# Kernel optimization log

Measured on AMD Instinct MI355X. Metric: run time of the kernel, lower is better.

## Reference

```python
import jax, jax.numpy as jnp
import numpy as np

ALPHA = 32.0 ** 2
EPS = 1e-5
SCALE = 64 ** (-0.5)  # dim_head ** -0.5
HEADS = 8


def stable_softmax(t, alpha=ALPHA):
    t = t / alpha
    t = t - jax.lax.stop_gradient(jnp.max(t, axis=-1, keepdims=True))
    return jax.nn.softmax(t * alpha, axis=-1)


def setup_inputs() -> dict:
    key = jax.random.key(0)
    k1, k2, k3 = jax.random.split(key, 3)
    dim, inner = 512, 8 * 64
    x = jax.random.normal(k1, (8, dim, 32, 32), dtype=jnp.float32)
    gamma = jnp.ones((1, dim, 1, 1), dtype=jnp.float32)
    # conv2d 1x1 weights, stored as [out_ch, in_ch]
    w_qkv = jax.random.normal(k2, (inner * 3, dim), dtype=jnp.float32) * (dim ** -0.5)
    w_out = jax.random.normal(k3, (dim, inner), dtype=jnp.float32) * (inner ** -0.5)
    return {"x": x, "gamma": gamma, "w_qkv": w_qkv, "w_out": w_out}


def reference(x, gamma, w_qkv, w_out):
    b, c, H, W = x.shape
    residual = x
    # LayerNormChan: normalize over channel dim (biased variance), scale by gamma
    mean = jnp.mean(x, axis=1, keepdims=True)
    var = jnp.var(x, axis=1, keepdims=True)
    xn = (x - mean) / jnp.sqrt(var + EPS) * gamma
    # 1x1 conv QKV projection
    qkv = jnp.einsum('oc,bchw->bohw', w_qkv, xn)
    q, k, v = jnp.split(qkv, 3, axis=1)
    n = H * W
    def to_heads(t):
        return t.reshape(b, HEADS, -1, n)  # b h c (x y)
    q, k, v = map(to_heads, (q, k, v))
    sim = jnp.einsum('bhci,bhcj->bhij', q, k) * SCALE
    attn = stable_softmax(sim)
    out = jnp.einsum('bhij,bhcj->bhci', attn, v)
    out = out.reshape(b, -1, H, W)  # b (h c) x y
    out = jnp.einsum('oc,bchw->bohw', w_out, out)
    return out + residual
```

## Files before the change

kernel.cpp:

```cpp
#include <hip/hip_runtime.h>
#include <hip/hip_bf16.h>

#define NDIM   512
#define NPOS   1024
#define NB     8
#define INNER  1536
#define DHEAD  64

typedef __attribute__((ext_vector_type(8))) short bf8v;
typedef __attribute__((ext_vector_type(4))) float f4v;

__device__ __forceinline__ f4v mfma16(bf8v a, bf8v b, f4v c) {
    return __builtin_amdgcn_mfma_f32_16x16x32_bf16(a, b, c, 0, 0, 0);
}

__device__ __forceinline__ unsigned short f2bs(float v) {
    __hip_bfloat16 h = __float2bfloat16(v);
    return *reinterpret_cast<unsigned short*>(&h);
}

__device__ __forceinline__ void gl_lds16(const unsigned short* g, unsigned short* l) {
    __builtin_amdgcn_global_load_lds(
        (const __attribute__((address_space(1))) void*)g,
        (__attribute__((address_space(3))) void*)l,
        16, 0, 0);
}

__global__ __launch_bounds__(256) void prep_kernel(
    const float* __restrict__ x, const float* __restrict__ gamma,
    const float* __restrict__ wq, const float* __restrict__ wo,
    unsigned short* __restrict__ xnT, unsigned short* __restrict__ wqb,
    unsigned short* __restrict__ wob)
{
    const int blk = blockIdx.x;
    const int t = threadIdx.x;
    if (blk >= 256) {
        const int n1 = INNER * NDIM / 4;
        int i = (blk - 256) * 256 + t;
        const float* src; unsigned short* dst; int j;
        if (i < n1) { src = wq; dst = wqb; j = i; }
        else        { src = wo; dst = wob; j = i - n1; }
        float4 v = ((const float4*)src)[j];
        ushort4 u;
        u.x = f2bs(v.x); u.y = f2bs(v.y); u.z = f2bs(v.z); u.w = f2bs(v.w);
        ((ushort4*)dst)[j] = u;
        return;
    }
    __shared__ float ssum[8][32];
    __shared__ float ssq[8][32];
    __shared__ float mean_s[32];
    __shared__ float rstd_s[32];
    __shared__ unsigned short tile[32][72];

    const int b = blk >> 5;
    const int n0 = (blk & 31) * 32;
    {
        const int ln = t & 31, cg = t >> 5;
        const float* xp = x + (size_t)b * NDIM * NPOS + n0 + ln;
        float s = 0.f, ss = 0.f;
#pragma unroll 8
        for (int c = cg * 64; c < cg * 64 + 64; ++c) {
            float v = xp[(size_t)c * NPOS];
            s += v; ss += v * v;
        }
        ssum[cg][ln] = s; ssq[cg][ln] = ss;
    }
    __syncthreads();
    if (t < 32) {
        float st = 0.f, sq = 0.f;
#pragma unroll
        for (int g = 0; g < 8; ++g) { st += ssum[g][t]; sq += ssq[g][t]; }
        float m = st * (1.0f / NDIM);
        float var = sq * (1.0f / NDIM) - m * m;
        mean_s[t] = m;
        rstd_s[t] = rsqrtf(var + 1e-5f);
    }
    __syncthreads();

    const int cl = t >> 2, nq = (t & 3) * 8;
    const int nr = t >> 3, ch = (t & 7) * 8;
    for (int c0 = 0; c0 < NDIM; c0 += 64) {
        const float g = gamma[c0 + cl];
        const float* xp = x + ((size_t)b * NDIM + c0 + cl) * NPOS + n0 + nq;
        float4 v0 = *(const float4*)(xp);
        float4 v1 = *(const float4*)(xp + 4);
        float4 m0 = *(const float4*)&mean_s[nq];
        float4 m1 = *(const float4*)&mean_s[nq + 4];
        float4 r0 = *(const float4*)&rstd_s[nq];
        float4 r1 = *(const float4*)&rstd_s[nq + 4];
        tile[nq + 0][cl] = f2bs((v0.x - m0.x) * r0.x * g);
        tile[nq + 1][cl] = f2bs((v0.y - m0.y) * r0.y * g);
        tile[nq + 2][cl] = f2bs((v0.z - m0.z) * r0.z * g);
        tile[nq + 3][cl] = f2bs((v0.w - m0.w) * r0.w * g);
        tile[nq + 4][cl] = f2bs((v1.x - m1.x) * r1.x * g);
        tile[nq + 5][cl] = f2bs((v1.y - m1.y) * r1.y * g);
        tile[nq + 6][cl] = f2bs((v1.z - m1.z) * r1.z * g);
        tile[nq + 7][cl] = f2bs((v1.w - m1.w) * r1.w * g);
        __syncthreads();
        unsigned short* dst = xnT + ((size_t)b * NPOS + n0 + nr) * NDIM + c0 + ch;
        *(uint4*)dst = *(const uint4*)&tile[nr][ch];
        __syncthreads();
    }
}

__global__ __launch_bounds__(256) void qkv_mfma_kernel(
    const unsigned short* __restrict__ wq, const unsigned short* __restrict__ xnT,
    unsigned short* __restrict__ qT, unsigned short* __restrict__ kT,
    unsigned short* __restrict__ vv)
{
    __shared__ __align__(16) unsigned short smem[4 * 64 * 72];

    const int b = blockIdx.z;
    const int m0 = blockIdx.y * 128, n0 = blockIdx.x * 128;
    const int t = threadIdx.x, w = t >> 6, lane = t & 63;
    const int l15 = lane & 15, quad = lane >> 4;
    const int wm = (w >> 1) * 64, wn = (w & 1) * 64;
    const unsigned short* Abase = wq + (size_t)m0 * NDIM;
    const unsigned short* Bbase = xnT + ((size_t)b * NPOS + n0) * NDIM;

    const int rl = lane >> 2, sl = lane & 3;
    const int cw = (sl ^ ((rl >> 1) & 3)) * 8;
    const int sA = (quad ^ ((l15 >> 1) & 3)) * 8;

    f4v acc[4][4];
#pragma unroll
    for (int i = 0; i < 4; ++i)
#pragma unroll
        for (int j = 0; j < 4; ++j) { acc[i][j][0]=0.f; acc[i][j][1]=0.f; acc[i][j][2]=0.f; acc[i][j][3]=0.f; }

#pragma unroll
    for (int e = 0; e < 2; ++e) {
        const int seg = w * 2 + e;
        const int r = seg * 16 + rl;
        gl_lds16(Abase + (size_t)r * NDIM + cw, smem + seg * 512);
        gl_lds16(Bbase + (size_t)r * NDIM + cw, smem + 4096 + seg * 512);
    }

    for (int k0 = 0; k0 < NDIM; k0 += 32) {
        const int cur = (k0 >> 5) & 1;
        unsigned short* At = smem + cur * 8192;
        unsigned short* Bt = At + 4096;
        __syncthreads();
        if (k0 + 32 < NDIM) {
            unsigned short* An = smem + (cur ^ 1) * 8192;
#pragma unroll
            for (int e = 0; e < 2; ++e) {
                const int seg = w * 2 + e;
                const int r = seg * 16 + rl;
                gl_lds16(Abase + (size_t)r * NDIM + k0 + 32 + cw, An + seg * 512);
                gl_lds16(Bbase + (size_t)r * NDIM + k0 + 32 + cw, An + 4096 + seg * 512);
            }
        }
        bf8v af[4], bfr[4];
#pragma unroll
        for (int ms = 0; ms < 4; ++ms) af[ms]  = *(const bf8v*)&At[(wm + ms * 16 + l15) * 32 + sA];
#pragma unroll
        for (int ns = 0; ns < 4; ++ns) bfr[ns] = *(const bf8v*)&Bt[(wn + ns * 16 + l15) * 32 + sA];
#pragma unroll
        for (int ms = 0; ms < 4; ++ms)
#pragma unroll
            for (int ns = 0; ns < 4; ++ns)
                acc[ms][ns] = mfma16(af[ms], bfr[ns], acc[ms][ns]);
    }
    __syncthreads();

    const int sec = m0 >> 9;
    const int om  = m0 & 511;
    if (sec == 2) {
        unsigned short (*bw)[72] = (unsigned short(*)[72])(smem + w * 64 * 72);
        unsigned short* vbase = vv + ((size_t)b * NDIM + om) * NPOS + n0;
#pragma unroll
        for (int ms = 0; ms < 4; ++ms)
#pragma unroll
            for (int ns = 0; ns < 4; ++ns)
#pragma unroll
                for (int r = 0; r < 4; ++r)
                    bw[ms * 16 + quad * 4 + r][ns * 16 + l15] = f2bs(acc[ms][ns][r]);
#pragma unroll
        for (int r2 = 0; r2 < 4; ++r2) {
            const int ml = r2 * 16 + (lane >> 2);
            unsigned short* dstr = vbase + (size_t)(wm + ml) * NPOS + wn + (lane & 3) * 8;
            *(uint4*)dstr        = *(const uint4*)&bw[ml][(lane & 3) * 8];
            *(uint4*)(dstr + 32) = *(const uint4*)&bw[ml][32 + (lane & 3) * 8];
        }
    } else {
        const float qsc = (sec == 0) ? 0.18033688f : 1.0f;
        unsigned short* gT = (sec == 0 ? qT : kT) + ((size_t)b * NPOS + n0) * NDIM + om;
        unsigned short (*bw)[72] = (unsigned short(*)[72])(smem + w * 64 * 72);
#pragma unroll
        for (int ms = 0; ms < 4; ++ms)
#pragma unroll
            for (int ns = 0; ns < 4; ++ns)
#pragma unroll
                for (int r = 0; r < 4; ++r)
                    bw[ns * 16 + l15][ms * 16 + quad * 4 + r] = f2bs(acc[ms][ns][r] * qsc);
#pragma unroll
        for (int r2 = 0; r2 < 4; ++r2) {
            const int nl = r2 * 16 + (lane >> 2);
            unsigned short* dstr = gT + (size_t)(wn + nl) * NDIM + wm + (lane & 3) * 8;
            *(uint4*)dstr        = *(const uint4*)&bw[nl][(lane & 3) * 8];
            *(uint4*)(dstr + 32) = *(const uint4*)&bw[nl][32 + (lane & 3) * 8];
        }
    }
}

__global__ __launch_bounds__(256, 2) void attn_mfma8_kernel(
    const unsigned short* __restrict__ qT, const unsigned short* __restrict__ kT,
    const unsigned short* __restrict__ vv, unsigned short* __restrict__ attnT)
{
    __shared__ __align__(16) unsigned short Kb[2][4096];
    __shared__ __align__(16) unsigned short Vb[2][4096];
    __shared__ __align__(16) unsigned short Ps[4][32][72];

    const int blk = blockIdx.x;
    const int xg = blk & 7, rr = blk >> 3;
    const int i0 = (rr & 7) * 128;
    const int bh = ((rr >> 3) << 3) | xg;
    const int b = bh >> 3, h = bh & 7;

    const int t = threadIdx.x, w = t >> 6, lane = t & 63;
    const int l15 = lane & 15, quad = lane >> 4;

    const unsigned short* kbase = kT + (size_t)b * NPOS * NDIM + h * DHEAD;
    const unsigned short* vbase = vv + ((size_t)b * NDIM + h * DHEAD) * NPOS;

    bf8v bq[2][2];
#pragma unroll
    for (int g = 0; g < 2; ++g) {
        const unsigned short* qrow =
            qT + ((size_t)b * NPOS + i0 + w * 32 + g * 16 + l15) * NDIM + h * DHEAD;
        bq[g][0] = *(const bf8v*)(qrow + quad * 8);
        bq[g][1] = *(const bf8v*)(qrow + 32 + quad * 8);
    }

    bf8v bones;
#pragma unroll
    for (int e = 0; e < 8; ++e) bones[e] = (short)0x3F80;

    const int rloc = lane >> 3;
    const int gch = ((lane & 7) ^ (rloc & 7)) * 8;
    const int sw0 = (quad ^ (l15 & 7)) * 8;
    const int sw1 = ((4 + quad) ^ (l15 & 7)) * 8;

#pragma unroll
    for (int e = 0; e < 2; ++e) {
        const int seg = w * 2 + e;
        const int row = seg * 8 + rloc;
        gl_lds16(kbase + (size_t)row * NDIM + gch, &Kb[0][seg * 512]);
        gl_lds16(vbase + (size_t)row * NPOS + gch, &Vb[0][seg * 512]);
    }

    f4v oc[2][5];
#pragma unroll
    for (int mg = 0; mg < 2; ++mg)
#pragma unroll
        for (int cs = 0; cs < 5; ++cs) { oc[mg][cs][0]=0.f; oc[mg][cs][1]=0.f; oc[mg][cs][2]=0.f; oc[mg][cs][3]=0.f; }

#pragma unroll 2
    for (int j0 = 0; j0 < NPOS; j0 += 64) {
        const int cur = (j0 >> 6) & 1, nxt = cur ^ 1;
        __syncthreads();
        if (j0 + 64 < NPOS) {
#pragma unroll
            for (int e = 0; e < 2; ++e) {
                const int seg = w * 2 + e;
                const int row = seg * 8 + rloc;
                gl_lds16(kbase + (size_t)(j0 + 64 + row) * NDIM + gch, &Kb[nxt][seg * 512]);
                gl_lds16(vbase + (size_t)row * NPOS + j0 + 64 + gch, &Vb[nxt][seg * 512]);
            }
        }

        f4v sacc[4][2];
        __builtin_amdgcn_s_setprio(1);
#pragma unroll
        for (int jt = 0; jt < 4; ++jt) {
            const int krow = (jt * 16 + l15) * 64;
            bf8v ak0 = *(const bf8v*)&Kb[cur][krow + sw0];
            bf8v ak1 = *(const bf8v*)&Kb[cur][krow + sw1];
#pragma unroll
            for (int g = 0; g < 2; ++g) {
                f4v s; s[0]=0.f; s[1]=0.f; s[2]=0.f; s[3]=0.f;
                s = mfma16(ak0, bq[g][0], s);
                sacc[jt][g] = mfma16(ak1, bq[g][1], s);
            }
        }
        __builtin_amdgcn_s_setprio(0);

#pragma unroll
        for (int jt = 0; jt < 4; ++jt)
#pragma unroll
            for (int g = 0; g < 2; ++g) {
                ushort4 pu;
                pu.x = f2bs(__builtin_amdgcn_exp2f(sacc[jt][g][0]));
                pu.y = f2bs(__builtin_amdgcn_exp2f(sacc[jt][g][1]));
                pu.z = f2bs(__builtin_amdgcn_exp2f(sacc[jt][g][2]));
                pu.w = f2bs(__builtin_amdgcn_exp2f(sacc[jt][g][3]));
                *(ushort4*)&Ps[w][g * 16 + l15][jt * 16 + quad * 4] = pu;
            }

        bf8v ap[2][2];
#pragma unroll
        for (int mg = 0; mg < 2; ++mg) {
            ap[mg][0] = *(const bf8v*)&Ps[w][mg * 16 + l15][quad * 8];
            ap[mg][1] = *(const bf8v*)&Ps[w][mg * 16 + l15][32 + quad * 8];
        }
        __builtin_amdgcn_s_setprio(1);
#pragma unroll
        for (int cs = 0; cs < 4; ++cs) {
            const int vrow = (cs * 16 + l15) * 64;
            bf8v bv0 = *(const bf8v*)&Vb[cur][vrow + sw0];
            bf8v bv1 = *(const bf8v*)&Vb[cur][vrow + sw1];
#pragma unroll
            for (int mg = 0; mg < 2; ++mg) {
                oc[mg][cs] = mfma16(ap[mg][0], bv0, oc[mg][cs]);
                oc[mg][cs] = mfma16(ap[mg][1], bv1, oc[mg][cs]);
            }
        }
#pragma unroll
        for (int mg = 0; mg < 2; ++mg) {
            oc[mg][4] = mfma16(ap[mg][0], bones, oc[mg][4]);
            oc[mg][4] = mfma16(ap[mg][1], bones, oc[mg][4]);
        }
        __builtin_amdgcn_s_setprio(0);
    }

#pragma unroll
    for (int mg = 0; mg < 2; ++mg) {
        float inv[4];
#pragma unroll
        for (int r = 0; r < 4; ++r) inv[r] = __builtin_amdgcn_rcpf(oc[mg][4][r]);
#pragma unroll
        for (int cs = 0; cs < 4; ++cs)
#pragma unroll
            for (int r = 0; r < 4; ++r)
                Ps[w][mg * 16 + quad * 4 + r][cs * 16 + l15] = f2bs(oc[mg][cs][r] * inv[r]);
    }
    {
        const int br = lane >> 1;
        const int bc = lane & 1;
        unsigned short* dst =
            attnT + ((size_t)b * NPOS + i0 + w * 32 + br) * NDIM + h * DHEAD;
#pragma unroll
        for (int q2 = 0; q2 < 4; ++q2)
            *(uint4*)(dst + (q2 * 2 + bc) * 8) = *(const uint4*)&Ps[w][br][(q2 * 2 + bc) * 8];
    }
}

__global__ __launch_bounds__(256) void out_mfma_kernel(
    const unsigned short* __restrict__ wo, const unsigned short* __restrict__ attnT,
    const float* __restrict__ x, float* __restrict__ outp)
{
    __shared__ __align__(16) unsigned short smem[12288];

    const int b = blockIdx.z;
    const int m0 = blockIdx.y * 64, n0 = blockIdx.x * 128;
    const int t = threadIdx.x, w = t >> 6, lane = t & 63;
    const int l15 = lane & 15, quad = lane >> 4;
    const int wm = (w >> 1) * 32, wn = (w & 1) * 64;
    const unsigned short* Abase = wo + (size_t)m0 * NDIM;
    const unsigned short* Bbase = attnT + ((size_t)b * NPOS + n0) * NDIM;

    const int rl = lane >> 2, sl = lane & 3;
    const int cw = (sl ^ ((rl >> 1) & 3)) * 8;
    const int sA = (quad ^ ((l15 >> 1) & 3)) * 8;

    f4v acc[2][4];
#pragma unroll
    for (int i = 0; i < 2; ++i)
#pragma unroll
        for (int j = 0; j < 4; ++j) { acc[i][j][0]=0.f; acc[i][j][1]=0.f; acc[i][j][2]=0.f; acc[i][j][3]=0.f; }

    {
        const int r = w * 16 + rl;
        gl_lds16(Abase + (size_t)r * NDIM + cw, smem + w * 512);
#pragma unroll
        for (int e = 0; e < 2; ++e) {
            const int seg = w * 2 + e;
            const int rb = seg * 16 + rl;
            gl_lds16(Bbase + (size_t)rb * NDIM + cw, smem + 2048 + seg * 512);
        }
    }

    for (int k0 = 0; k0 < NDIM; k0 += 32) {
        const int cur = (k0 >> 5) & 1;
        unsigned short* At = smem + cur * 6144;
        unsigned short* Bt = At + 2048;
        __syncthreads();
        if (k0 + 32 < NDIM) {
            unsigned short* An = smem + (cur ^ 1) * 6144;
            const int r = w * 16 + rl;
            gl_lds16(Abase + (size_t)r * NDIM + k0 + 32 + cw, An + w * 512);
#pragma unroll
            for (int e = 0; e < 2; ++e) {
                const int seg = w * 2 + e;
                const int rb = seg * 16 + rl;
                gl_lds16(Bbase + (size_t)rb * NDIM + k0 + 32 + cw, An + 2048 + seg * 512);
            }
        }
        bf8v af[2], bfr[4];
#pragma unroll
        for (int ms = 0; ms < 2; ++ms) af[ms]  = *(const bf8v*)&At[(wm + ms * 16 + l15) * 32 + sA];
#pragma unroll
        for (int ns = 0; ns < 4; ++ns) bfr[ns] = *(const bf8v*)&Bt[(wn + ns * 16 + l15) * 32 + sA];
#pragma unroll
        for (int ms = 0; ms < 2; ++ms)
#pragma unroll
            for (int ns = 0; ns < 4; ++ns)
                acc[ms][ns] = mfma16(af[ms], bfr[ns], acc[ms][ns]);
    }
    const float* xb = x + ((size_t)b * NDIM + m0) * NPOS + n0;
    float* ob = outp + ((size_t)b * NDIM + m0) * NPOS + n0;
#pragma unroll
    for (int ms = 0; ms < 2; ++ms)
#pragma unroll
        for (int r = 0; r < 4; ++r) {
            int m = wm + ms * 16 + quad * 4 + r;
#pragma unroll
            for (int ns = 0; ns < 4; ++ns) {
                int n = wn + ns * 16 + l15;
                ob[(size_t)m * NPOS + n] = acc[ms][ns][r] + xb[(size_t)m * NPOS + n];
            }
        }
}

extern "C" void kernel_launch(void* const* d_in, const int* in_sizes, int n_in,
                              void* d_out, int out_size, void* d_ws, size_t ws_size,
                              hipStream_t stream) {
    const float* x     = (const float*)d_in[0];
    const float* gamma = (const float*)d_in[1];
    const float* w_qkv = (const float*)d_in[2];
    const float* w_out = (const float*)d_in[3];
    float* out = (float*)d_out;

    unsigned short* xnT = (unsigned short*)d_ws;
    unsigned short* wqb = xnT + (size_t)NB * NPOS * NDIM;
    unsigned short* wob = wqb + (size_t)INNER * NDIM;
    unsigned short* qTw = wob + (size_t)NDIM * NDIM;
    unsigned short* kTw = qTw + (size_t)NB * NPOS * NDIM;
    unsigned short* vvw = kTw + (size_t)NB * NPOS * NDIM;
    unsigned short* aTw = vvw + (size_t)NB * NPOS * NDIM;

    prep_kernel<<<256 + (INNER * NDIM + NDIM * NDIM) / 4 / 256, 256, 0, stream>>>(
        x, gamma, w_qkv, w_out, xnT, wqb, wob);
    qkv_mfma_kernel<<<dim3(NPOS / 128, INNER / 128, NB), 256, 0, stream>>>(
        wqb, xnT, qTw, kTw, vvw);
    attn_mfma8_kernel<<<512, 256, 0, stream>>>(qTw, kTw, vvw, aTw);
    out_mfma_kernel<<<dim3(NPOS / 128, NDIM / 64, NB), 256, 0, stream>>>(wob, aTw, x, out);
}
```

Baseline: 133.8 us.

## Fuse all four stages into one cooperative persistent kernel with grid syncs

Replaces four separate kernel launches (layernorm/weight conversion, QKV GEMM, attention, output projection) with one cooperative kernel of 512 blocks that loops over each stage's work items and separates stages with grid.sync(). The goal is to remove launch gaps and tail idle time between kernels. In exchange, occupancy is capped at 2 blocks per CU, the QKV stage runs 768 tiles on 512 blocks, which leaves an imbalanced second wave, and each grid barrier has a cost. It falls back to the old multi-kernel path if the cooperative launch fails.

```diff
diff --git a/kernel.cpp b/kernel.cpp
--- a/kernel.cpp
+++ b/kernel.cpp
@@ -1,5 +1,8 @@
 #include <hip/hip_runtime.h>
 #include <hip/hip_bf16.h>
+#include <hip/hip_cooperative_groups.h>
+
+namespace cg = cooperative_groups;
 
 #define NDIM   512
 #define NPOS   1024
@@ -25,6 +28,413 @@
         (__attribute__((address_space(3))) void*)l,
         16, 0, 0);
 }
+
+__global__ __launch_bounds__(256, 2) void mega_kernel(
+    const float* __restrict__ x, const float* __restrict__ gamma,
+    const float* __restrict__ wq32, const float* __restrict__ wo32,
+    unsigned short* __restrict__ xnT, unsigned short* __restrict__ wqb,
+    unsigned short* __restrict__ wob, unsigned short* __restrict__ qT,
+    unsigned short* __restrict__ kT, unsigned short* __restrict__ vv,
+    unsigned short* __restrict__ attnT, float* __restrict__ outp)
+{
+    __shared__ __align__(16) unsigned char SM[51200];
+    cg::grid_group grid = cg::this_grid();
+    const int t = threadIdx.x;
+
+    {
+        float* ssum   = (float*)SM;
+        float* ssq    = (float*)(SM + 1024);
+        float* mean_s = (float*)(SM + 2048);
+        float* rstd_s = (float*)(SM + 2176);
+        unsigned short (*tile)[72] = (unsigned short(*)[72])(SM + 2304);
+        for (int vb = blockIdx.x; vb < 1280; vb += 512) {
+            if (vb >= 256) {
+                const int n1 = INNER * NDIM / 4;
+                int i = (vb - 256) * 256 + t;
+                const float* src; unsigned short* dst; int j;
+                if (i < n1) { src = wq32; dst = wqb; j = i; }
+                else        { src = wo32; dst = wob; j = i - n1; }
+                float4 v = ((const float4*)src)[j];
+                ushort4 u;
+                u.x = f2bs(v.x); u.y = f2bs(v.y); u.z = f2bs(v.z); u.w = f2bs(v.w);
+                ((ushort4*)dst)[j] = u;
+                continue;
+            }
+            const int b = vb >> 5;
+            const int n0 = (vb & 31) * 32;
+            {
+                const int ln = t & 31, cgp = t >> 5;
+                const float* xp = x + (size_t)b * NDIM * NPOS + n0 + ln;
+                float s = 0.f, ss = 0.f;
+#pragma unroll 8
+                for (int c = cgp * 64; c < cgp * 64 + 64; ++c) {
+                    float v = xp[(size_t)c * NPOS];
+                    s += v; ss += v * v;
+                }
+                ssum[cgp * 32 + ln] = s; ssq[cgp * 32 + ln] = ss;
+            }
+            __syncthreads();
+            if (t < 32) {
+                float st = 0.f, sq = 0.f;
+#pragma unroll
+                for (int g = 0; g < 8; ++g) { st += ssum[g * 32 + t]; sq += ssq[g * 32 + t]; }
+                float m = st * (1.0f / NDIM);
+                float var = sq * (1.0f / NDIM) - m * m;
+                mean_s[t] = m;
+                rstd_s[t] = rsqrtf(var + 1e-5f);
+            }
+            __syncthreads();
+
+            const int cl = t >> 2, nq = (t & 3) * 8;
+            const int nr = t >> 3, ch = (t & 7) * 8;
+            for (int c0 = 0; c0 < NDIM; c0 += 64) {
+                const float g = gamma[c0 + cl];
+                const float* xp = x + ((size_t)b * NDIM + c0 + cl) * NPOS + n0 + nq;
+                float4 v0 = *(const float4*)(xp);
+                float4 v1 = *(const float4*)(xp + 4);
+                float4 m0 = *(const float4*)&mean_s[nq];
+                float4 m1 = *(const float4*)&mean_s[nq + 4];
+                float4 r0 = *(const float4*)&rstd_s[nq];
+                float4 r1 = *(const float4*)&rstd_s[nq + 4];
+                tile[nq + 0][cl] = f2bs((v0.x - m0.x) * r0.x * g);
+                tile[nq + 1][cl] = f2bs((v0.y - m0.y) * r0.y * g);
+                tile[nq + 2][cl] = f2bs((v0.z - m0.z) * r0.z * g);
+                tile[nq + 3][cl] = f2bs((v0.w - m0.w) * r0.w * g);
+                tile[nq + 4][cl] = f2bs((v1.x - m1.x) * r1.x * g);
+                tile[nq + 5][cl] = f2bs((v1.y - m1.y) * r1.y * g);
+                tile[nq + 6][cl] = f2bs((v1.z - m1.z) * r1.z * g);
+                tile[nq + 7][cl] = f2bs((v1.w - m1.w) * r1.w * g);
+                __syncthreads();
+                unsigned short* dst = xnT + ((size_t)b * NPOS + n0 + nr) * NDIM + c0 + ch;
+                *(uint4*)dst = *(const uint4*)&tile[nr][ch];
+                __syncthreads();
+            }
+        }
+    }
+    grid.sync();
+
+    {
+        unsigned short* smem = (unsigned short*)SM;
+        const int w = t >> 6, lane = t & 63;
+        const int l15 = lane & 15, quad = lane >> 4;
+        const int wm = (w >> 1) * 64, wn = (w & 1) * 64;
+        const int rl = lane >> 2, sl = lane & 3;
+        const int cw = (sl ^ ((rl >> 1) & 3)) * 8;
+        const int sA = (quad ^ ((l15 >> 1) & 3)) * 8;
+
+        for (int vb = blockIdx.x; vb < 768; vb += 512) {
+            __syncthreads();
+            const int n0 = (vb & 7) * 128;
+            const int mi = vb >> 3;
+            const int b  = mi / 12;
+            const int m0 = (mi - b * 12) * 128;
+            const unsigned short* Abase = wqb + (size_t)m0 * NDIM;
+            const unsigned short* Bbase = xnT + ((size_t)b * NPOS + n0) * NDIM;
+
+            f4v acc[4][4];
+#pragma unroll
+            for (int i = 0; i < 4; ++i)
+#pragma unroll
+                for (int j = 0; j < 4; ++j) { acc[i][j][0]=0.f; acc[i][j][1]=0.f; acc[i][j][2]=0.f; acc[i][j][3]=0.f; }
+
+#pragma unroll
+            for (int e = 0; e < 2; ++e) {
+                const int seg = w * 2 + e;
+                const int r = seg * 16 + rl;
+                gl_lds16(Abase + (size_t)r * NDIM + cw, smem + seg * 512);
+                gl_lds16(Bbase + (size_t)r * NDIM + cw, smem + 4096 + seg * 512);
+            }
+
+            for (int k0 = 0; k0 < NDIM; k0 += 32) {
+                const int cur = (k0 >> 5) & 1;
+                unsigned short* At = smem + cur * 8192;
+                unsigned short* Bt = At + 4096;
+                __syncthreads();
+                if (k0 + 32 < NDIM) {
+                    unsigned short* An = smem + (cur ^ 1) * 8192;
+#pragma unroll
+                    for (int e = 0; e < 2; ++e) {
+                        const int seg = w * 2 + e;
+                        const int r = seg * 16 + rl;
+                        gl_lds16(Abase + (size_t)r * NDIM + k0 + 32 + cw, An + seg * 512);
+                        gl_lds16(Bbase + (size_t)r * NDIM + k0 + 32 + cw, An + 4096 + seg * 512);
+                    }
+                }
+                bf8v af[4], bfr[4];
+#pragma unroll
+                for (int ms = 0; ms < 4; ++ms) af[ms]  = *(const bf8v*)&At[(wm + ms * 16 + l15) * 32 + sA];
+#pragma unroll
+                for (int ns = 0; ns < 4; ++ns) bfr[ns] = *(const bf8v*)&Bt[(wn + ns * 16 + l15) * 32 + sA];
+#pragma unroll
+                for (int ms = 0; ms < 4; ++ms)
+#pragma unroll
+                    for (int ns = 0; ns < 4; ++ns)
+                        acc[ms][ns] = mfma16(af[ms], bfr[ns], acc[ms][ns]);
+            }
+            __syncthreads();
+
+            const int sec = m0 >> 9;
+            const int om  = m0 & 511;
+            if (sec == 2) {
+                unsigned short (*bw)[72] = (unsigned short(*)[72])(smem + w * 64 * 72);
+                unsigned short* vbase = vv + ((size_t)b * NDIM + om) * NPOS + n0;
+#pragma unroll
+                for (int ms = 0; ms < 4; ++ms)
+#pragma unroll
+                    for (int ns = 0; ns < 4; ++ns)
+#pragma unroll
+                        for (int r = 0; r < 4; ++r)
+                            bw[ms * 16 + quad * 4 + r][ns * 16 + l15] = f2bs(acc[ms][ns][r]);
+#pragma unroll
+                for (int r2 = 0; r2 < 4; ++r2) {
+                    const int ml = r2 * 16 + (lane >> 2);
+                    unsigned short* dstr = vbase + (size_t)(wm + ml) * NPOS + wn + (lane & 3) * 8;
+                    *(uint4*)dstr        = *(const uint4*)&bw[ml][(lane & 3) * 8];
+                    *(uint4*)(dstr + 32) = *(const uint4*)&bw[ml][32 + (lane & 3) * 8];
+                }
+            } else {
+                const float qsc = (sec == 0) ? 0.18033688f : 1.0f;
+                unsigned short* gT = (sec == 0 ? qT : kT) + ((size_t)b * NPOS + n0) * NDIM + om;
+                unsigned short (*bw)[72] = (unsigned short(*)[72])(smem + w * 64 * 72);
+#pragma unroll
+                for (int ms = 0; ms < 4; ++ms)
+#pragma unroll
+                    for (int ns = 0; ns < 4; ++ns)
+#pragma unroll
+                        for (int r = 0; r < 4; ++r)
+                            bw[ns * 16 + l15][ms * 16 + quad * 4 + r] = f2bs(acc[ms][ns][r] * qsc);
+#pragma unroll
+                for (int r2 = 0; r2 < 4; ++r2) {
+                    const int nl = r2 * 16 + (lane >> 2);
+                    unsigned short* dstr = gT + (size_t)(wn + nl) * NDIM + wm + (lane & 3) * 8;
+                    *(uint4*)dstr        = *(const uint4*)&bw[nl][(lane & 3) * 8];
+                    *(uint4*)(dstr + 32) = *(const uint4*)&bw[nl][32 + (lane & 3) * 8];
+                }
+            }
+        }
+    }
+    grid.sync();
+
+    {
+        unsigned short* KbB = (unsigned short*)SM;
+        unsigned short* VbB = (unsigned short*)(SM + 16384);
+        unsigned short (*Ps)[32][72] = (unsigned short(*)[32][72])(SM + 32768);
+
+        const int blk = blockIdx.x;
+        const int xg = blk & 7, rr = blk >> 3;
+        const int i0 = (rr & 7) * 128;
+        const int bh = ((rr >> 3) << 3) | xg;
+        const int b = bh >> 3, h = bh & 7;
+
+        const int w = t >> 6, lane = t & 63;
+        const int l15 = lane & 15, quad = lane >> 4;
+
+        const unsigned short* kbase = kT + (size_t)b * NPOS * NDIM + h * DHEAD;
+        const unsigned short* vbase = vv + ((size_t)b * NDIM + h * DHEAD) * NPOS;
+
+        bf8v bq[2][2];
+#pragma unroll
+        for (int g = 0; g < 2; ++g) {
+            const unsigned short* qrow =
+                qT + ((size_t)b * NPOS + i0 + w * 32 + g * 16 + l15) * NDIM + h * DHEAD;
+            bq[g][0] = *(const bf8v*)(qrow + quad * 8);
+            bq[g][1] = *(const bf8v*)(qrow + 32 + quad * 8);
+        }
+
+        bf8v bones;
+#pragma unroll
+        for (int e = 0; e < 8; ++e) bones[e] = (short)0x3F80;
+
+        const int rloc = lane >> 3;
+        const int gch = ((lane & 7) ^ (rloc & 7)) * 8;
+        const int sw0 = (quad ^ (l15 & 7)) * 8;
+        const int sw1 = ((4 + quad) ^ (l15 & 7)) * 8;
+
+#pragma unroll
+        for (int e = 0; e < 2; ++e) {
+            const int seg = w * 2 + e;
+            const int row = seg * 8 + rloc;
+            gl_lds16(kbase + (size_t)row * NDIM + gch, KbB + seg * 512);
+            gl_lds16(vbase + (size_t)row * NPOS + gch, VbB + seg * 512);
+        }
+
+        f4v oc[2][5];
+#pragma unroll
+        for (int mg = 0; mg < 2; ++mg)
+#pragma unroll
+            for (int cs = 0; cs < 5; ++cs) { oc[mg][cs][0]=0.f; oc[mg][cs][1]=0.f; oc[mg][cs][2]=0.f; oc[mg][cs][3]=0.f; }
+
+#pragma unroll 2
+        for (int j0 = 0; j0 < NPOS; j0 += 64) {
+            const int cur = (j0 >> 6) & 1, nxt = cur ^ 1;
+            unsigned short* Kc = KbB + cur * 4096;
+            unsigned short* Vc = VbB + cur * 4096;
+            __syncthreads();
+            if (j0 + 64 < NPOS) {
+#pragma unroll
+                for (int e = 0; e < 2; ++e) {
+                    const int seg = w * 2 + e;
+                    const int row = seg * 8 + rloc;
+                    gl_lds16(kbase + (size_t)(j0 + 64 + row) * NDIM + gch, KbB + nxt * 4096 + seg * 512);
+                    gl_lds16(vbase + (size_t)row * NPOS + j0 + 64 + gch, VbB + nxt * 4096 + seg * 512);
+                }
+            }
+
+            f4v sacc[4][2];
+            __builtin_amdgcn_s_setprio(1);
+#pragma unroll
+            for (int jt = 0; jt < 4; ++jt) {
+                const int krow = (jt * 16 + l15) * 64;
+                bf8v ak0 = *(const bf8v*)&Kc[krow + sw0];
+                bf8v ak1 = *(const bf8v*)&Kc[krow + sw1];
+#pragma unroll
+                for (int g = 0; g < 2; ++g) {
+                    f4v s; s[0]=0.f; s[1]=0.f; s[2]=0.f; s[3]=0.f;
+                    s = mfma16(ak0, bq[g][0], s);
+                    sacc[jt][g] = mfma16(ak1, bq[g][1], s);
+                }
+            }
+            __builtin_amdgcn_s_setprio(0);
+
+#pragma unroll
+            for (int jt = 0; jt < 4; ++jt)
+#pragma unroll
+                for (int g = 0; g < 2; ++g) {
+                    ushort4 pu;
+                    pu.x = f2bs(__builtin_amdgcn_exp2f(sacc[jt][g][0]));
+                    pu.y = f2bs(__builtin_amdgcn_exp2f(sacc[jt][g][1]));
+                    pu.z = f2bs(__builtin_amdgcn_exp2f(sacc[jt][g][2]));
+                    pu.w = f2bs(__builtin_amdgcn_exp2f(sacc[jt][g][3]));
+                    *(ushort4*)&Ps[w][g * 16 + l15][jt * 16 + quad * 4] = pu;
+                }
+
+            bf8v ap[2][2];
+#pragma unroll
+            for (int mg = 0; mg < 2; ++mg) {
+                ap[mg][0] = *(const bf8v*)&Ps[w][mg * 16 + l15][quad * 8];
+                ap[mg][1] = *(const bf8v*)&Ps[w][mg * 16 + l15][32 + quad * 8];
+            }
+            __builtin_amdgcn_s_setprio(1);
+#pragma unroll
+            for (int cs = 0; cs < 4; ++cs) {
+                const int vrow = (cs * 16 + l15) * 64;
+                bf8v bv0 = *(const bf8v*)&Vc[vrow + sw0];
+                bf8v bv1 = *(const bf8v*)&Vc[vrow + sw1];
+#pragma unroll
+                for (int mg = 0; mg < 2; ++mg) {
+                    oc[mg][cs] = mfma16(ap[mg][0], bv0, oc[mg][cs]);
+                    oc[mg][cs] = mfma16(ap[mg][1], bv1, oc[mg][cs]);
+                }
+            }
+#pragma unroll
+            for (int mg = 0; mg < 2; ++mg) {
+                oc[mg][4] = mfma16(ap[mg][0], bones, oc[mg][4]);
+                oc[mg][4] = mfma16(ap[mg][1], bones, oc[mg][4]);
+            }
+            __builtin_amdgcn_s_setprio(0);
+        }
+
+#pragma unroll
+        for (int mg = 0; mg < 2; ++mg) {
+            float inv[4];
+#pragma unroll
+            for (int r = 0; r < 4; ++r) inv[r] = __builtin_amdgcn_rcpf(oc[mg][4][r]);
+#pragma unroll
+            for (int cs = 0; cs < 4; ++cs)
+#pragma unroll
+                for (int r = 0; r < 4; ++r)
+                    Ps[w][mg * 16 + quad * 4 + r][cs * 16 + l15] = f2bs(oc[mg][cs][r] * inv[r]);
+        }
+        {
+            const int br = lane >> 1;
+            const int bc = lane & 1;
+            unsigned short* dst =
+                attnT + ((size_t)b * NPOS + i0 + w * 32 + br) * NDIM + h * DHEAD;
+#pragma unroll
+            for (int q2 = 0; q2 < 4; ++q2)
+                *(uint4*)(dst + (q2 * 2 + bc) * 8) = *(const uint4*)&Ps[w][br][(q2 * 2 + bc) * 8];
+        }
+    }
+    grid.sync();
+
+    {
+        unsigned short* smem = (unsigned short*)SM;
+
+        const int vb = blockIdx.x;
+        const int n0 = (vb & 7) * 128;
+        const int m0 = ((vb >> 3) & 7) * 64;
+        const int b  = vb >> 6;
+
+        const int w = t >> 6, lane = t & 63;
+        const int l15 = lane & 15, quad = lane >> 4;
+        const int wm = (w >> 1) * 32, wn = (w & 1) * 64;
+        const unsigned short* Abase = wob + (size_t)m0 * NDIM;
+        const unsigned short* Bbase = attnT + ((size_t)b * NPOS + n0) * NDIM;
+
+        const int rl = lane >> 2, sl = lane & 3;
+        const int cw = (sl ^ ((rl >> 1) & 3)) * 8;
+        const int sA = (quad ^ ((l15 >> 1) & 3)) * 8;
+
+        f4v acc[2][4];
+#pragma unroll
+        for (int i = 0; i < 2; ++i)
+#pragma unroll
+            for (int j = 0; j < 4; ++j) { acc[i][j][0]=0.f; acc[i][j][1]=0.f; acc[i][j][2]=0.f; acc[i][j][3]=0.f; }
+
+        {
+            const int r = w * 16 + rl;
+            gl_lds16(Abase + (size_t)r * NDIM + cw, smem + w * 512);
+#pragma unroll
+            for (int e = 0; e < 2; ++e) {
+                const int seg = w * 2 + e;
+                const int rb = seg * 16 + rl;
+                gl_lds16(Bbase + (size_t)rb * NDIM + cw, smem + 2048 + seg * 512);
+            }
+        }
+
+        for (int k0 = 0; k0 < NDIM; k0 += 32) {
+            const int cur = (k0 >> 5) & 1;
+            unsigned short* At = smem + cur * 6144;
+            unsigned short* Bt = At + 2048;
+            __syncthreads();
+            if (k0 + 32 < NDIM) {
+                unsigned short* An = smem + (cur ^ 1) * 6144;
+                const int r = w * 16 + rl;
+                gl_lds16(Abase + (size_t)r * NDIM + k0 + 32 + cw, An + w * 512);
+#pragma unroll
+                for (int e = 0; e < 2; ++e) {
+                    const int seg = w * 2 + e;
+                    const int rb = seg * 16 + rl;
+                    gl_lds16(Bbase + (size_t)rb * NDIM + k0 + 32 + cw, An + 2048 + seg * 512);
+                }
+            }
+            bf8v af[2], bfr[4];
+#pragma unroll
+            for (int ms = 0; ms < 2; ++ms) af[ms]  = *(const bf8v*)&At[(wm + ms * 16 + l15) * 32 + sA];
+#pragma unroll
+            for (int ns = 0; ns < 4; ++ns) bfr[ns] = *(const bf8v*)&Bt[(wn + ns * 16 + l15) * 32 + sA];
+#pragma unroll
+            for (int ms = 0; ms < 2; ++ms)
+#pragma unroll
+                for (int ns = 0; ns < 4; ++ns)
+                    acc[ms][ns] = mfma16(af[ms], bfr[ns], acc[ms][ns]);
+        }
+        const float* xb = x + ((size_t)b * NDIM + m0) * NPOS + n0;
+        float* ob = outp + ((size_t)b * NDIM + m0) * NPOS + n0;
+#pragma unroll
+        for (int ms = 0; ms < 2; ++ms)
+#pragma unroll
+            for (int r = 0; r < 4; ++r) {
+                int m = wm + ms * 16 + quad * 4 + r;
+#pragma unroll
+                for (int ns = 0; ns < 4; ++ns) {
+                    int n = wn + ns * 16 + l15;
+                    ob[(size_t)m * NPOS + n] = acc[ms][ns][r] + xb[(size_t)m * NPOS + n];
+                }
+            }
+    }
+}
+
 
 __global__ __launch_bounds__(256) void prep_kernel(
     const float* __restrict__ x, const float* __restrict__ gamma,
@@ -440,10 +850,18 @@
     unsigned short* vvw = kTw + (size_t)NB * NPOS * NDIM;
     unsigned short* aTw = vvw + (size_t)NB * NPOS * NDIM;
 
-    prep_kernel<<<256 + (INNER * NDIM + NDIM * NDIM) / 4 / 256, 256, 0, stream>>>(
-        x, gamma, w_qkv, w_out, xnT, wqb, wob);
-    qkv_mfma_kernel<<<dim3(NPOS / 128, INNER / 128, NB), 256, 0, stream>>>(
-        wqb, xnT, qTw, kTw, vvw);
-    attn_mfma8_kernel<<<512, 256, 0, stream>>>(qTw, kTw, vvw, aTw);
-    out_mfma_kernel<<<dim3(NPOS / 128, NDIM / 64, NB), 256, 0, stream>>>(wob, aTw, x, out);
+    void* args[] = {
+        (void*)&x, (void*)&gamma, (void*)&w_qkv, (void*)&w_out,
+        (void*)&xnT, (void*)&wqb, (void*)&wob, (void*)&qTw,
+        (void*)&kTw, (void*)&vvw, (void*)&aTw, (void*)&out };
+    hipError_t err = hipLaunchCooperativeKernel(
+        mega_kernel, dim3(512), dim3(256), args, 0, stream);
+    if (err != hipSuccess) {
+        prep_kernel<<<256 + (INNER * NDIM + NDIM * NDIM) / 4 / 256, 256, 0, stream>>>(
+            x, gamma, w_qkv, w_out, xnT, wqb, wob);
+        qkv_mfma_kernel<<<dim3(NPOS / 128, INNER / 128, NB), 256, 0, stream>>>(
+            wqb, xnT, qTw, kTw, vvw);
+        attn_mfma8_kernel<<<512, 256, 0, stream>>>(qTw, kTw, vvw, aTw);
+        out_mfma_kernel<<<dim3(NPOS / 128, NDIM / 64, NB), 256, 0, stream>>>(wob, aTw, x, out);
+    }
 }
```

Measured after the change: 327.1 us. 2.44x slower.

## Triple-buffer LDS loads in QKV and output GEMMs with partial vmcnt waits

Applied to the files above, without the earlier changes.

Switches the QKV and output projection GEMM main loops from double to triple buffering in LDS. Two K-tiles are prefetched, and explicit s_waitcnt vmcnt counts let only the oldest async global-to-LDS loads complete before each barrier. The loop is also fully unrolled. This is meant to hide global load latency better, at the cost of more shared memory per block, which may lower occupancy. It also relies on exact vmcnt counting matching the number of outstanding loads.

```diff
diff --git a/kernel.cpp b/kernel.cpp
--- a/kernel.cpp
+++ b/kernel.cpp
@@ -108,7 +108,7 @@
     unsigned short* __restrict__ qT, unsigned short* __restrict__ kT,
     unsigned short* __restrict__ vv)
 {
-    __shared__ __align__(16) unsigned short smem[4 * 64 * 72];
+    __shared__ __align__(16) unsigned short smem[3 * 8192];
 
     const int b = blockIdx.z;
     const int m0 = blockIdx.y * 128, n0 = blockIdx.x * 128;
@@ -128,29 +128,29 @@
 #pragma unroll
         for (int j = 0; j < 4; ++j) { acc[i][j][0]=0.f; acc[i][j][1]=0.f; acc[i][j][2]=0.f; acc[i][j][3]=0.f; }
 
-#pragma unroll
-    for (int e = 0; e < 2; ++e) {
-        const int seg = w * 2 + e;
-        const int r = seg * 16 + rl;
-        gl_lds16(Abase + (size_t)r * NDIM + cw, smem + seg * 512);
-        gl_lds16(Bbase + (size_t)r * NDIM + cw, smem + 4096 + seg * 512);
-    }
-
-    for (int k0 = 0; k0 < NDIM; k0 += 32) {
-        const int cur = (k0 >> 5) & 1;
-        unsigned short* At = smem + cur * 8192;
+    auto STAGE = [&](int k0, unsigned short* buf) {
+#pragma unroll
+        for (int e = 0; e < 2; ++e) {
+            const int seg = w * 2 + e;
+            const int r = seg * 16 + rl;
+            gl_lds16(Abase + (size_t)r * NDIM + k0 + cw, buf + seg * 512);
+            gl_lds16(Bbase + (size_t)r * NDIM + k0 + cw, buf + 4096 + seg * 512);
+        }
+    };
+
+    STAGE(0, smem);
+    STAGE(32, smem + 8192);
+
+#pragma unroll
+    for (int kt = 0; kt < 16; ++kt) {
+        if (kt < 15) asm volatile("s_waitcnt vmcnt(4)" ::: "memory");
+        else         asm volatile("s_waitcnt vmcnt(0)" ::: "memory");
+        __builtin_amdgcn_sched_barrier(0);
+        __builtin_amdgcn_s_barrier();
+        __builtin_amdgcn_sched_barrier(0);
+        if (kt + 2 < 16) STAGE((kt + 2) * 32, smem + ((kt + 2) % 3) * 8192);
+        unsigned short* At = smem + (kt % 3) * 8192;
         unsigned short* Bt = At + 4096;
-        __syncthreads();
-        if (k0 + 32 < NDIM) {
-            unsigned short* An = smem + (cur ^ 1) * 8192;
-#pragma unroll
-            for (int e = 0; e < 2; ++e) {
-                const int seg = w * 2 + e;
-                const int r = seg * 16 + rl;
-                gl_lds16(Abase + (size_t)r * NDIM + k0 + 32 + cw, An + seg * 512);
-                gl_lds16(Bbase + (size_t)r * NDIM + k0 + 32 + cw, An + 4096 + seg * 512);
-            }
-        }
         bf8v af[4], bfr[4];
 #pragma unroll
         for (int ms = 0; ms < 4; ++ms) af[ms]  = *(const bf8v*)&At[(wm + ms * 16 + l15) * 32 + sA];
@@ -350,7 +350,7 @@
     const unsigned short* __restrict__ wo, const unsigned short* __restrict__ attnT,
     const float* __restrict__ x, float* __restrict__ outp)
 {
-    __shared__ __align__(16) unsigned short smem[12288];
+    __shared__ __align__(16) unsigned short smem[3 * 6144];
 
     const int b = blockIdx.z;
     const int m0 = blockIdx.y * 64, n0 = blockIdx.x * 128;
@@ -370,33 +370,30 @@
 #pragma unroll
         for (int j = 0; j < 4; ++j) { acc[i][j][0]=0.f; acc[i][j][1]=0.f; acc[i][j][2]=0.f; acc[i][j][3]=0.f; }
 
-    {
+    auto STAGE = [&](int k0, unsigned short* buf) {
         const int r = w * 16 + rl;
-        gl_lds16(Abase + (size_t)r * NDIM + cw, smem + w * 512);
+        gl_lds16(Abase + (size_t)r * NDIM + k0 + cw, buf + w * 512);
 #pragma unroll
         for (int e = 0; e < 2; ++e) {
             const int seg = w * 2 + e;
             const int rb = seg * 16 + rl;
-            gl_lds16(Bbase + (size_t)rb * NDIM + cw, smem + 2048 + seg * 512);
-        }
-    }
-
-    for (int k0 = 0; k0 < NDIM; k0 += 32) {
-        const int cur = (k0 >> 5) & 1;
-        unsigned short* At = smem + cur * 6144;
+            gl_lds16(Bbase + (size_t)rb * NDIM + k0 + cw, buf + 2048 + seg * 512);
+        }
+    };
+
+    STAGE(0, smem);
+    STAGE(32, smem + 6144);
+
+#pragma unroll
+    for (int kt = 0; kt < 16; ++kt) {
+        if (kt < 15) asm volatile("s_waitcnt vmcnt(3)" ::: "memory");
+        else         asm volatile("s_waitcnt vmcnt(0)" ::: "memory");
+        __builtin_amdgcn_sched_barrier(0);
+        __builtin_amdgcn_s_barrier();
+        __builtin_amdgcn_sched_barrier(0);
+        if (kt + 2 < 16) STAGE((kt + 2) * 32, smem + ((kt + 2) % 3) * 6144);
+        unsigned short* At = smem + (kt % 3) * 6144;
         unsigned short* Bt = At + 2048;
-        __syncthreads();
-        if (k0 + 32 < NDIM) {
-            unsigned short* An = smem + (cur ^ 1) * 6144;
-            const int r = w * 16 + rl;
-            gl_lds16(Abase + (size_t)r * NDIM + k0 + 32 + cw, An + w * 512);
-#pragma unroll
-            for (int e = 0; e < 2; ++e) {
-                const int seg = w * 2 + e;
-                const int rb = seg * 16 + rl;
-                gl_lds16(Bbase + (size_t)rb * NDIM + k0 + 32 + cw, An + 2048 + seg * 512);
-            }
-        }
         bf8v af[2], bfr[4];
 #pragma unroll
         for (int ms = 0; ms < 2; ++ms) af[ms]  = *(const bf8v*)&At[(wm + ms * 16 + l15) * 32 + sA];
```

Result: no change. 132.1 us (-1.2%).
